# Optimization experiments

Hardware: AMD Instinct MI355X
Metric: run time of the kernel (lower is better)

## Reference

```python
import jax, jax.numpy as jnp
import numpy as np

HEAD_DIM = 104  # 1664 / 16
NUM_HEADS = 16
THETA = 10000.0
# per-coordinate rotary sub-dims: dim//3, dim//3, remainder
_DIMS = [HEAD_DIM // 3, HEAD_DIM // 3, HEAD_DIM - 2 * (HEAD_DIM // 3)]  # [34, 34, 36]
_INV_FREQS = [jnp.asarray(1.0 / THETA ** (np.arange(0, d, 2, dtype=np.float32) / d)) for d in _DIMS]


def _rotate_half(x):
    x1, x2 = jnp.split(x, 2, axis=-1)
    return jnp.concatenate([-x2, x1], axis=-1)


def _rope_cos_sin(coords):
    # coords: [B, N, 3] -> emb [B, N, HEAD_DIM]
    parts = []
    for i in range(3):
        f = coords[:, :, i:i + 1].astype(jnp.float32) * _INV_FREQS[i]  # [B,N,d_i/2]
        parts.append(jnp.concatenate([f, f], axis=-1))  # [B,N,d_i]
    emb = jnp.concatenate(parts, axis=-1)  # [B,N,HEAD_DIM]
    return jnp.cos(emb), jnp.sin(emb)


def setup_inputs() -> dict:
    key = jax.random.key(0)
    ks = jax.random.split(key, 6)
    B, N, C = 2, 2048, 1664
    s = 0.02
    return {
        "x": jax.random.normal(ks[0], (B, N, C), jnp.float32),
        "coords": jax.random.randint(ks[1], (B, N, 3), 0, 64, jnp.int32),
        "qkv_w": jax.random.normal(ks[2], (C, 3 * C), jnp.float32) * s,
        "qkv_b": jax.random.normal(ks[3], (3 * C,), jnp.float32) * s,
        "proj_w": jax.random.normal(ks[4], (C, C), jnp.float32) * s,
        "proj_b": jax.random.normal(ks[5], (C,), jnp.float32) * s,
    }


def reference(x, coords, qkv_w, qkv_b, proj_w, proj_b):
    B, N, C = x.shape
    H, D = NUM_HEADS, HEAD_DIM
    scale = D ** -0.5

    qkv = (x @ qkv_w + qkv_b).reshape(B, N, 3, H, D)
    q, k, v = qkv[:, :, 0], qkv[:, :, 1], qkv[:, :, 2]  # [B,N,H,D]

    cos, sin = _rope_cos_sin(coords)  # [B,N,D]
    cos = cos[:, :, None, :]
    sin = sin[:, :, None, :]
    q = q * cos + _rotate_half(q) * sin
    k = k * cos + _rotate_half(k) * sin

    attn = jnp.einsum("bnhd,bmhd->bhnm", q, k) * scale
    attn = jax.nn.softmax(attn, axis=-1)
    out = jnp.einsum("bhnm,bmhd->bnhd", attn, v).reshape(B, N, C)
    return out @ proj_w + proj_b
```

## Files before the change

kernel.cpp:

```cpp
#include <hip/hip_runtime.h>
#include <hip/hip_bf16.h>
#include <cstdint>

typedef __bf16 bf16;
typedef bf16 bf16x8 __attribute__((ext_vector_type(8)));
typedef bf16 bf16x4 __attribute__((ext_vector_type(4)));
typedef float f32x4 __attribute__((ext_vector_type(4)));

__device__ __forceinline__ void gl_lds16(const bf16* g, bf16* l) {
    __builtin_amdgcn_global_load_lds((const __attribute__((address_space(1))) void*)g,
                                     (__attribute__((address_space(3))) void*)l, 16, 0, 0);
}

__global__ __launch_bounds__(256) void k_pre(const float* __restrict__ x, bf16* __restrict__ xb,
                                             const float* __restrict__ qkv_w, bf16* __restrict__ wqkvT,
                                             const float* __restrict__ proj_w, bf16* __restrict__ wprojT,
                                             const int* __restrict__ coords,
                                             float* __restrict__ cosT, float* __restrict__ sinT) {
    __shared__ float tile[32][33];
    int bid = blockIdx.x, t = threadIdx.x;
    if (bid < 6656) {
        int i = bid * 256 + t;
        f32x4 v = *(const f32x4*)(x + (size_t)i * 4);
        bf16x4 o = { (bf16)v[0], (bf16)v[1], (bf16)v[2], (bf16)v[3] };
        *(bf16x4*)(xb + (size_t)i * 4) = o;
    } else if (bid < 17472) {
        const float* in; bf16* outp; int K, Nn, b2;
        if (bid < 14768) { b2 = bid - 6656;  in = qkv_w;  outp = wqkvT;  K = 1664; Nn = 4992; }
        else             { b2 = bid - 14768; in = proj_w; outp = wprojT; K = 1664; Nn = 1664; }
        int bx = b2 % 52, by = b2 / 52;
        int k0 = bx * 32, n0 = by * 32;
        int tx = t & 31, ty = t >> 5;
#pragma unroll
        for (int i = 0; i < 4; i++)
            tile[ty + i * 8][tx] = in[(size_t)(k0 + ty + i * 8) * Nn + n0 + tx];
        __syncthreads();
#pragma unroll
        for (int i = 0; i < 4; i++)
            outp[(size_t)(n0 + ty + i * 8) * K + k0 + tx] = (bf16)tile[tx][ty + i * 8];
    } else {
        int idx = (bid - 17472) * 256 + t;
        if (idx < 212992) {
            int bn = idx / 52, p = idx - bn * 52;
            int which = (p < 17) ? 0 : (p < 34 ? 1 : 2);
            int c = coords[bn * 3 + which];
            int j, base, half; float dpv;
            if (p < 17)      { j = p;      base = 0;  half = 17; dpv = 34.f; }
            else if (p < 34) { j = p - 17; base = 34; half = 17; dpv = 34.f; }
            else             { j = p - 34; base = 68; half = 18; dpv = 36.f; }
            float inv = __expf(-2.0f * (float)j / dpv * 9.210340371976184f);
            float a = (float)c * inv;
            float sn, cs;
            __sincosf(a, &sn, &cs);
            size_t o1 = (size_t)bn * 104 + base + j;
            size_t o2 = o1 + half;
            cosT[o1] = cs; cosT[o2] = cs;
            sinT[o1] = sn; sinT[o2] = sn;
        }
    }
}

template <int FM, int FN, bool OUT_BF16>
__global__ __launch_bounds__(256) void k_gemm(const bf16* __restrict__ A, const bf16* __restrict__ BT,
                                              const float* __restrict__ bias, void* __restrict__ Cout,
                                              int M, int Nn, int K) {
    constexpr int BM = FM * 32, BN = FN * 32;
    __shared__ __align__(16) bf16 aT[BM * 64];
    __shared__ __align__(16) bf16 bT[BN * 64];
    int n0 = blockIdx.x * BN;
    if (n0 >= Nn) return;
    int m0 = blockIdx.y * BM;
    int t = threadIdx.x;
    int w = t >> 6, l = t & 63, quad = l >> 4, lc = l & 15;
    int wm = (w >> 1) * (FM * 16), wn = (w & 1) * (FN * 16);
    f32x4 acc[FM][FN] = {};
    for (int k0 = 0; k0 < K; k0 += 64) {
#pragma unroll
        for (int it = 0; it < FM; it++) {
            int s = it * 256 + t;
            int r = s >> 3, sc = s & 7;
            gl_lds16(A + (size_t)(m0 + r) * K + k0 + (sc ^ (r & 7)) * 8, aT + s * 8);
        }
#pragma unroll
        for (int it = 0; it < FN; it++) {
            int s = it * 256 + t;
            int r = s >> 3, sc = s & 7;
            gl_lds16(BT + (size_t)(n0 + r) * K + k0 + (sc ^ (r & 7)) * 8, bT + s * 8);
        }
        __syncthreads();
#pragma unroll
        for (int sub = 0; sub < 2; sub++) {
            bf16x8 af[FM], bfr[FN];
#pragma unroll
            for (int i = 0; i < FM; i++) {
                int ra = wm + i * 16 + lc;
                af[i] = *(const bf16x8*)(aT + ra * 64 + ((sub * 4 + quad) ^ (ra & 7)) * 8);
            }
#pragma unroll
            for (int j = 0; j < FN; j++) {
                int rb = wn + j * 16 + lc;
                bfr[j] = *(const bf16x8*)(bT + rb * 64 + ((sub * 4 + quad) ^ (rb & 7)) * 8);
            }
#pragma unroll
            for (int i = 0; i < FM; i++)
#pragma unroll
                for (int j = 0; j < FN; j++)
                    acc[i][j] = __builtin_amdgcn_mfma_f32_16x16x32_bf16(af[i], bfr[j], acc[i][j], 0, 0, 0);
        }
        __syncthreads();
    }
#pragma unroll
    for (int i = 0; i < FM; i++)
#pragma unroll
        for (int j = 0; j < FN; j++) {
            int col = n0 + wn + j * 16 + lc;
            float bv = bias[col];
#pragma unroll
            for (int r = 0; r < 4; r++) {
                int row = m0 + wm + i * 16 + quad * 4 + r;
                float v = acc[i][j][r] + bv;
                if (OUT_BF16) ((bf16*)Cout)[(size_t)row * Nn + col] = (bf16)v;
                else          ((float*)Cout)[(size_t)row * Nn + col] = v;
            }
        }
}

__global__ __launch_bounds__(256) void k_mid(const bf16* __restrict__ qkv, const float* __restrict__ cosT,
                                             const float* __restrict__ sinT, bf16* __restrict__ qp,
                                             bf16* __restrict__ kp, bf16* __restrict__ vt) {
    __shared__ bf16 tile[32][33];
    int bid = blockIdx.x, t = threadIdx.x;
    if (bid < 256) {
        int idx = bid * 256 + t;
        int h = idx & 15, n = (idx >> 4) & 2047, b = idx >> 15;
        int bn = b * 2048 + n;
        const bf16* qrow = qkv + (size_t)bn * 4992 + h * 104;
        const bf16* krow = qrow + 1664;
        const float* co = cosT + (size_t)bn * 104;
        const float* si = sinT + (size_t)bn * 104;
        int bh = b * 16 + h;
        bf16* qo = qp + ((size_t)bh * 2048 + n) * 128;
        bf16* ko = kp + ((size_t)bh * 2048 + n) * 128;
        const float scale = 0.14146788954942663f;
#pragma unroll
        for (int cc = 0; cc < 13; cc++) {
            int d = cc * 4;
            bf16x4 q1 = *(const bf16x4*)(qrow + d);
            bf16x4 q2 = *(const bf16x4*)(qrow + d + 52);
            bf16x4 k1 = *(const bf16x4*)(krow + d);
            bf16x4 k2 = *(const bf16x4*)(krow + d + 52);
            f32x4 c1 = *(const f32x4*)(co + d);
            f32x4 c2 = *(const f32x4*)(co + d + 52);
            f32x4 s1 = *(const f32x4*)(si + d);
            f32x4 s2 = *(const f32x4*)(si + d + 52);
            bf16x4 o1, o2, p1, p2;
#pragma unroll
            for (int i = 0; i < 4; i++) {
                float fq1 = (float)q1[i], fq2 = (float)q2[i];
                float fk1 = (float)k1[i], fk2 = (float)k2[i];
                o1[i] = (bf16)((fq1 * c1[i] - fq2 * s1[i]) * scale);
                o2[i] = (bf16)((fq2 * c2[i] + fq1 * s2[i]) * scale);
                p1[i] = (bf16)(fk1 * c1[i] - fk2 * s1[i]);
                p2[i] = (bf16)(fk2 * c2[i] + fk1 * s2[i]);
            }
            *(bf16x4*)(qo + d) = o1;
            *(bf16x4*)(qo + d + 52) = o2;
            *(bf16x4*)(ko + d) = p1;
            *(bf16x4*)(ko + d + 52) = p2;
        }
        bf16x8 z = {};
        *(bf16x8*)(qo + 104) = z; *(bf16x8*)(qo + 112) = z; *(bf16x8*)(qo + 120) = z;
        *(bf16x8*)(ko + 104) = z; *(bf16x8*)(ko + 112) = z; *(bf16x8*)(ko + 120) = z;
    } else {
        int b2 = bid - 256;
        int bh = b2 & 31, n0 = ((b2 >> 5) & 63) * 32, d0 = (b2 >> 11) * 32;
        int b = bh >> 4, h = bh & 15;
        int tx = t & 31, ty = t >> 5;
#pragma unroll
        for (int i = 0; i < 4; i++) {
            int n = n0 + ty + i * 8; int d = d0 + tx;
            bf16 v = (bf16)0.0f;
            if (d < 104)       v = qkv[(size_t)(b * 2048 + n) * 4992 + 3328 + h * 104 + d];
            else if (d == 104) v = (bf16)1.0f;
            tile[ty + i * 8][tx] = v;
        }
        __syncthreads();
        bf16* vto = vt + (size_t)bh * 128 * 2048;
#pragma unroll
        for (int i = 0; i < 4; i++) {
            int d = d0 + ty + i * 8; int n = n0 + tx;
            vto[(size_t)d * 2048 + n] = tile[tx][ty + i * 8];
        }
    }
}

__global__ __launch_bounds__(512, 4) void k_attn(const bf16* __restrict__ qp, const bf16* __restrict__ kp,
                                                 const bf16* __restrict__ vt, bf16* __restrict__ out) {
    __shared__ __align__(16) bf16 kT[64 * 128];
    __shared__ __align__(16) bf16 vT[128 * 64];
    __shared__ __align__(16) bf16 pS[8][16 * 72];
    int t = threadIdx.x;
    int bh = blockIdx.x, qt = blockIdx.y;
    int w = t >> 6, l = t & 63, quad = l >> 4, lc = l & 15;
    const bf16* Q  = qp + (size_t)bh * 2048 * 128;
    const bf16* Kb = kp + (size_t)bh * 2048 * 128;
    const bf16* Vb = vt + (size_t)bh * 128 * 2048;
    int wq = qt * 128 + w * 16;
    bf16* pSw = pS[w];

    bf16x8 qf[4];
#pragma unroll
    for (int kc = 0; kc < 4; kc++)
        qf[kc] = *(const bf16x8*)(Q + (size_t)(wq + lc) * 128 + kc * 32 + quad * 8);

    f32x4 accO[7] = {};

    for (int kv0 = 0; kv0 < 2048; kv0 += 64) {
#pragma unroll
        for (int it = 0; it < 2; it++) {
            int s = it * 512 + t;
            int key = s >> 4;
            int dc = (s & 15) ^ (key & 15);
            gl_lds16(Kb + (size_t)(kv0 + key) * 128 + dc * 8, kT + s * 8);
            int d = s >> 3;
            int kc = (s & 7) ^ (d & 7);
            gl_lds16(Vb + (size_t)d * 2048 + kv0 + kc * 8, vT + s * 8);
        }
        __syncthreads();

        f32x4 sf[4] = {};
#pragma unroll
        for (int ns = 0; ns < 4; ns++) {
            int key = ns * 16 + lc;
#pragma unroll
            for (int kc = 0; kc < 4; kc++) {
                int slot = key * 16 + ((kc * 4 + quad) ^ lc);
                bf16x8 kf = *(const bf16x8*)(kT + slot * 8);
                sf[ns] = __builtin_amdgcn_mfma_f32_16x16x32_bf16(kf, qf[kc], sf[ns], 0, 0, 0);
            }
        }
#pragma unroll
        for (int ns = 0; ns < 4; ns++) {
            bf16x4 pk;
#pragma unroll
            for (int r = 0; r < 4; r++)
                pk[r] = (bf16)exp2f(sf[ns][r]);
            *(bf16x4*)(pSw + lc * 72 + ns * 16 + quad * 4) = pk;
        }
        asm volatile("s_waitcnt lgkmcnt(0)" ::: "memory");
        bf16x8 pb[2];
#pragma unroll
        for (int ks = 0; ks < 2; ks++)
            pb[ks] = *(const bf16x8*)(pSw + lc * 72 + ks * 32 + quad * 8);
#pragma unroll
        for (int ks = 0; ks < 2; ks++)
#pragma unroll
            for (int nd = 0; nd < 7; nd++) {
                int d = nd * 16 + lc;
                int slot = d * 8 + ((ks * 4 + quad) ^ (d & 7));
                bf16x8 vf = *(const bf16x8*)(vT + slot * 8);
                accO[nd] = __builtin_amdgcn_mfma_f32_16x16x32_bf16(vf, pb[ks], accO[nd], 0, 0, 0);
            }
        __syncthreads();
    }

    float lsum = __shfl(accO[6][0], 32 + lc);
    float invl = 1.0f / lsum;
    int b = bh >> 4, h = bh & 15;
    int qrow = wq + lc;
    bf16* orow = out + (size_t)(b * 2048 + qrow) * 1664 + h * 104;
#pragma unroll
    for (int nd = 0; nd < 7; nd++) {
        int d0 = nd * 16 + quad * 4;
        if (d0 < 104) {
            f32x4 v = accO[nd];
            bf16x4 o = { (bf16)(v[0] * invl), (bf16)(v[1] * invl),
                         (bf16)(v[2] * invl), (bf16)(v[3] * invl) };
            *(bf16x4*)(orow + d0) = o;
        }
    }
}

extern "C" void kernel_launch(void* const* d_in, const int* in_sizes, int n_in,
                              void* d_out, int out_size, void* d_ws, size_t ws_size,
                              hipStream_t stream) {
    const float* x      = (const float*)d_in[0];
    const int*   coords = (const int*)d_in[1];
    const float* qkv_w  = (const float*)d_in[2];
    const float* qkv_b  = (const float*)d_in[3];
    const float* proj_w = (const float*)d_in[4];
    const float* proj_b = (const float*)d_in[5];
    float* out = (float*)d_out;
    uint8_t* ws = (uint8_t*)d_ws;

    constexpr size_t SZ_XB    = 4096ull * 1664 * 2;
    constexpr size_t SZ_WQKV  = 4992ull * 1664 * 2;
    constexpr size_t SZ_WPROJ = 1664ull * 1664 * 2;
    constexpr size_t SZ_QKV   = 4096ull * 4992 * 2;
    constexpr size_t SZ_QPAD  = 32ull * 2048 * 128 * 2;
    constexpr size_t SZ_CS    = 4096ull * 104 * 4;

    size_t o_xb    = 0;
    size_t o_wqkv  = o_xb + SZ_XB;
    size_t o_wproj = o_wqkv + SZ_WQKV;
    size_t o_qkv   = o_wproj + SZ_WPROJ;
    size_t o_kpad  = o_qkv + SZ_QKV;
    size_t o_vt    = o_kpad + SZ_QPAD;
    size_t o_cos   = o_vt + SZ_QPAD;
    size_t o_sin   = o_cos + SZ_CS;
    size_t o_qpad  = 0;
    size_t o_attn  = o_qkv;

    bf16* xb     = (bf16*)(ws + o_xb);
    bf16* wqkvT  = (bf16*)(ws + o_wqkv);
    bf16* wprojT = (bf16*)(ws + o_wproj);
    bf16* qkvb   = (bf16*)(ws + o_qkv);
    bf16* qpad   = (bf16*)(ws + o_qpad);
    bf16* kpad   = (bf16*)(ws + o_kpad);
    bf16* vtpad  = (bf16*)(ws + o_vt);
    float* cosT  = (float*)(ws + o_cos);
    float* sinT  = (float*)(ws + o_sin);
    bf16* attno  = (bf16*)(ws + o_attn);

    k_pre<<<18304, 256, 0, stream>>>(x, xb, qkv_w, wqkvT, proj_w, wprojT, coords, cosT, sinT);
    k_gemm<4, 4, true><<<dim3(40, 32), 256, 0, stream>>>(xb, wqkvT, qkv_b, (void*)qkvb, 4096, 4992, 1664);
    k_mid<<<8448, 256, 0, stream>>>(qkvb, cosT, sinT, qpad, kpad, vtpad);
    k_attn<<<dim3(32, 16), 512, 0, stream>>>(qpad, kpad, vtpad, attno);
    k_gemm<2, 4, false><<<dim3(16, 64), 256, 0, stream>>>(attno, wprojT, proj_b, (void*)out, 4096, 1664, 1664);
}
```

Baseline: 370.8 us.

## Process two query tiles per wave in attention to reuse K/V fragments

The attention kernel now uses 4 waves of 256 threads per block, each wave handling 32 query rows as two 16-row MFMA tiles instead of 16 rows. Each K and V fragment read from LDS feeds two MFMAs, halving LDS reads per unit of compute. This doubles accumulator and query registers per wave and halves waves per block, which may reduce occupancy and latency hiding. Launch bounds change to (256,3) and each thread now issues four async loads per tile instead of two.

```diff
diff --git a/kernel.cpp b/kernel.cpp
--- a/kernel.cpp
+++ b/kernel.cpp
@@ -194,31 +194,33 @@
     }
 }
 
-__global__ __launch_bounds__(512, 4) void k_attn(const bf16* __restrict__ qp, const bf16* __restrict__ kp,
+__global__ __launch_bounds__(256, 3) void k_attn(const bf16* __restrict__ qp, const bf16* __restrict__ kp,
                                                  const bf16* __restrict__ vt, bf16* __restrict__ out) {
     __shared__ __align__(16) bf16 kT[64 * 128];
     __shared__ __align__(16) bf16 vT[128 * 64];
-    __shared__ __align__(16) bf16 pS[8][16 * 72];
+    __shared__ __align__(16) bf16 pS[4][32 * 72];
     int t = threadIdx.x;
     int bh = blockIdx.x, qt = blockIdx.y;
     int w = t >> 6, l = t & 63, quad = l >> 4, lc = l & 15;
     const bf16* Q  = qp + (size_t)bh * 2048 * 128;
     const bf16* Kb = kp + (size_t)bh * 2048 * 128;
     const bf16* Vb = vt + (size_t)bh * 128 * 2048;
-    int wq = qt * 128 + w * 16;
+    int wq = qt * 128 + w * 32;
     bf16* pSw = pS[w];
 
-    bf16x8 qf[4];
-#pragma unroll
-    for (int kc = 0; kc < 4; kc++)
-        qf[kc] = *(const bf16x8*)(Q + (size_t)(wq + lc) * 128 + kc * 32 + quad * 8);
-
-    f32x4 accO[7] = {};
+    bf16x8 qf[2][4];
+#pragma unroll
+    for (int nq = 0; nq < 2; nq++)
+#pragma unroll
+        for (int kc = 0; kc < 4; kc++)
+            qf[nq][kc] = *(const bf16x8*)(Q + (size_t)(wq + nq * 16 + lc) * 128 + kc * 32 + quad * 8);
+
+    f32x4 accO[2][7] = {};
 
     for (int kv0 = 0; kv0 < 2048; kv0 += 64) {
 #pragma unroll
-        for (int it = 0; it < 2; it++) {
-            int s = it * 512 + t;
+        for (int it = 0; it < 4; it++) {
+            int s = it * 256 + t;
             int key = s >> 4;
             int dc = (s & 15) ^ (key & 15);
             gl_lds16(Kb + (size_t)(kv0 + key) * 128 + dc * 8, kT + s * 8);
@@ -228,7 +230,7 @@
         }
         __syncthreads();
 
-        f32x4 sf[4] = {};
+        f32x4 sf[2][4] = {};
 #pragma unroll
         for (int ns = 0; ns < 4; ns++) {
             int key = ns * 16 + lc;
@@ -236,22 +238,27 @@
             for (int kc = 0; kc < 4; kc++) {
                 int slot = key * 16 + ((kc * 4 + quad) ^ lc);
                 bf16x8 kf = *(const bf16x8*)(kT + slot * 8);
-                sf[ns] = __builtin_amdgcn_mfma_f32_16x16x32_bf16(kf, qf[kc], sf[ns], 0, 0, 0);
-            }
-        }
-#pragma unroll
-        for (int ns = 0; ns < 4; ns++) {
-            bf16x4 pk;
-#pragma unroll
-            for (int r = 0; r < 4; r++)
-                pk[r] = (bf16)exp2f(sf[ns][r]);
-            *(bf16x4*)(pSw + lc * 72 + ns * 16 + quad * 4) = pk;
-        }
+                sf[0][ns] = __builtin_amdgcn_mfma_f32_16x16x32_bf16(kf, qf[0][kc], sf[0][ns], 0, 0, 0);
+                sf[1][ns] = __builtin_amdgcn_mfma_f32_16x16x32_bf16(kf, qf[1][kc], sf[1][ns], 0, 0, 0);
+            }
+        }
+#pragma unroll
+        for (int nq = 0; nq < 2; nq++)
+#pragma unroll
+            for (int ns = 0; ns < 4; ns++) {
+                bf16x4 pk;
+#pragma unroll
+                for (int r = 0; r < 4; r++)
+                    pk[r] = (bf16)exp2f(sf[nq][ns][r]);
+                *(bf16x4*)(pSw + (nq * 16 + lc) * 72 + ns * 16 + quad * 4) = pk;
+            }
         asm volatile("s_waitcnt lgkmcnt(0)" ::: "memory");
-        bf16x8 pb[2];
-#pragma unroll
-        for (int ks = 0; ks < 2; ks++)
-            pb[ks] = *(const bf16x8*)(pSw + lc * 72 + ks * 32 + quad * 8);
+        bf16x8 pb[2][2];
+#pragma unroll
+        for (int nq = 0; nq < 2; nq++)
+#pragma unroll
+            for (int ks = 0; ks < 2; ks++)
+                pb[nq][ks] = *(const bf16x8*)(pSw + (nq * 16 + lc) * 72 + ks * 32 + quad * 8);
 #pragma unroll
         for (int ks = 0; ks < 2; ks++)
 #pragma unroll
@@ -259,24 +266,28 @@
                 int d = nd * 16 + lc;
                 int slot = d * 8 + ((ks * 4 + quad) ^ (d & 7));
                 bf16x8 vf = *(const bf16x8*)(vT + slot * 8);
-                accO[nd] = __builtin_amdgcn_mfma_f32_16x16x32_bf16(vf, pb[ks], accO[nd], 0, 0, 0);
-            }
-        __syncthreads();
-    }
-
-    float lsum = __shfl(accO[6][0], 32 + lc);
-    float invl = 1.0f / lsum;
+                accO[0][nd] = __builtin_amdgcn_mfma_f32_16x16x32_bf16(vf, pb[0][ks], accO[0][nd], 0, 0, 0);
+                accO[1][nd] = __builtin_amdgcn_mfma_f32_16x16x32_bf16(vf, pb[1][ks], accO[1][nd], 0, 0, 0);
+            }
+        __syncthreads();
+    }
+
     int b = bh >> 4, h = bh & 15;
-    int qrow = wq + lc;
-    bf16* orow = out + (size_t)(b * 2048 + qrow) * 1664 + h * 104;
-#pragma unroll
-    for (int nd = 0; nd < 7; nd++) {
-        int d0 = nd * 16 + quad * 4;
-        if (d0 < 104) {
-            f32x4 v = accO[nd];
-            bf16x4 o = { (bf16)(v[0] * invl), (bf16)(v[1] * invl),
-                         (bf16)(v[2] * invl), (bf16)(v[3] * invl) };
-            *(bf16x4*)(orow + d0) = o;
+#pragma unroll
+    for (int nq = 0; nq < 2; nq++) {
+        float lsum = __shfl(accO[nq][6][0], 32 + lc);
+        float invl = 1.0f / lsum;
+        int qrow = wq + nq * 16 + lc;
+        bf16* orow = out + (size_t)(b * 2048 + qrow) * 1664 + h * 104;
+#pragma unroll
+        for (int nd = 0; nd < 7; nd++) {
+            int d0 = nd * 16 + quad * 4;
+            if (d0 < 104) {
+                f32x4 v = accO[nq][nd];
+                bf16x4 o = { (bf16)(v[0] * invl), (bf16)(v[1] * invl),
+                             (bf16)(v[2] * invl), (bf16)(v[3] * invl) };
+                *(bf16x4*)(orow + d0) = o;
+            }
         }
     }
 }
@@ -325,6 +336,6 @@
     k_pre<<<18304, 256, 0, stream>>>(x, xb, qkv_w, wqkvT, proj_w, wprojT, coords, cosT, sinT);
     k_gemm<4, 4, true><<<dim3(40, 32), 256, 0, stream>>>(xb, wqkvT, qkv_b, (void*)qkvb, 4096, 4992, 1664);
     k_mid<<<8448, 256, 0, stream>>>(qkvb, cosT, sinT, qpad, kpad, vtpad);
-    k_attn<<<dim3(32, 16), 512, 0, stream>>>(qpad, kpad, vtpad, attno);
+    k_attn<<<dim3(32, 16), 256, 0, stream>>>(qpad, kpad, vtpad, attno);
     k_gemm<2, 4, false><<<dim3(16, 64), 256, 0, stream>>>(attno, wprojT, proj_b, (void*)out, 4096, 1664, 1664);
 }
```

New measurement: 384.7 us. +3.8%, slower.
